# Kernel optimization log

Hardware: AMD Instinct MI355X
Metric: run time of the kernel (lower is better)

Reference implementation:

```python
import jax, jax.numpy as jnp
import numpy as np

NUM_NODES = 128
TEMPERATURE = 1.0
NEG = -1e30  # stand-in for -inf that is safe under softmax/grad


def setup_inputs() -> dict:
    key = jax.random.key(0)
    k1, k2, k3 = jax.random.split(key, 3)
    D, N = 1024, NUM_NODES
    P = jax.random.normal(k1, (N, N), jnp.float32)
    P = P.at[jnp.arange(N), jnp.arange(N)].set(-50.0)  # fill_diagonal_(-50)
    uniforms = jax.random.uniform(k2, (D, N), jnp.float32)       # categorical sampling draws
    gumbel_u = jax.random.uniform(k3, (D, 2, N, N), jnp.float32)  # gumbel-softmax base uniforms
    return {"P": P, "uniforms": uniforms, "gumbel_u": gumbel_u, "num_dags": D}


def reference(P, uniforms, gumbel_u, num_dags):
    N = P.shape[0]
    D = uniforms.shape[0]
    sigP = jax.nn.sigmoid(P)  # [N,N], shared across all dags

    # --- Phase 1: sequential node-ordering sampling (mask-based, fixed shapes) ---
    def step(active, u):
        # active: [D,N] bool, True = node still remaining
        masked = jnp.where(active[:, None, :], sigP[None, :, :], NEG)  # [D,N,N]
        row_max = masked.max(-1)                                       # max over remaining cols
        logits = jnp.where(active, (1.0 - row_max) / TEMPERATURE, NEG)
        probs = jax.nn.softmax(logits, axis=-1)                        # softmax over remaining rows
        cum = jnp.cumsum(probs, -1)
        cond = (cum >= u[:, None]) & active
        idx = jnp.argmax(cond, -1)
        last_active = (N - 1) - jnp.argmax(active[:, ::-1], -1)
        idx = jnp.where(cond.any(-1), idx, last_active)  # fp fallback
        active = active & (jnp.arange(N)[None, :] != idx[:, None])
        return active, idx

    active0 = jnp.ones((D, N), dtype=bool)
    _, order_T = jax.lax.scan(step, active0, uniforms.T)  # scan over N steps
    order = order_T.T  # [D,N]

    # --- Phase 2: permute, lower-triangular, gumbel-softmax, unpermute ---
    Ap = sigP[order[:, :, None], order[:, None, :]]  # [D,N,N] = sigP[order_i, order_j]
    tril_mask = jnp.tril(jnp.ones((N, N), dtype=bool), -1)
    A_low = jnp.where(tril_mask, Ap, 0.0)
    logA = jnp.where(tril_mask, jnp.log(jnp.where(tril_mask, Ap, 1.0)), NEG)
    log1mA = jnp.log1p(-A_low)
    logits2 = jnp.stack([logA, log1mA], axis=1)  # [D,2,N,N]
    g = -jnp.log(-jnp.log(gumbel_u + 1e-10) + 1e-10)
    y_soft = jax.nn.softmax(logits2 + g, axis=1)  # tau = 1 (torch default)
    am = jnp.argmax(y_soft, axis=1)  # [D,N,N]
    hard = (am[:, None, :, :] == jnp.arange(2)[None, :, None, None]).astype(y_soft.dtype)
    y = jax.lax.stop_gradient(hard - y_soft) + y_soft  # straight-through
    Y = y[:, 0]  # [D,N,N]

    # undo permutation: out[d, order[i], order[j]] = Y[d, i, j]
    inv = jnp.argsort(order, axis=-1)
    unperm = jax.vmap(lambda m, p: m[p][:, p])(Y, inv)
    return unperm.transpose(0, 2, 1), order
```

## Files before the change

kernel.cpp:

```cpp
#include <hip/hip_runtime.h>

#define NN 128
#define NEGF -1e30f
#define DELTA 1.5e-5f

__device__ __forceinline__ float dpp_scan_add(float x) {
    int v;
    v = __builtin_amdgcn_update_dpp(0, __float_as_int(x), 0x111, 0xf, 0xf, true);
    x += __int_as_float(v);
    v = __builtin_amdgcn_update_dpp(0, __float_as_int(x), 0x112, 0xf, 0xf, true);
    x += __int_as_float(v);
    v = __builtin_amdgcn_update_dpp(0, __float_as_int(x), 0x114, 0xf, 0xf, true);
    x += __int_as_float(v);
    v = __builtin_amdgcn_update_dpp(0, __float_as_int(x), 0x118, 0xf, 0xf, true);
    x += __int_as_float(v);
    v = __builtin_amdgcn_update_dpp(0, __float_as_int(x), 0x142, 0xa, 0xf, true);
    x += __int_as_float(v);
    v = __builtin_amdgcn_update_dpp(0, __float_as_int(x), 0x143, 0xc, 0xf, true);
    x += __int_as_float(v);
    return x;
}

__device__ __forceinline__ float dpp_scan_max(float x) {
    const int negi = __float_as_int(NEGF);
    int v;
    v = __builtin_amdgcn_update_dpp(negi, __float_as_int(x), 0x111, 0xf, 0xf, false);
    x = fmaxf(x, __int_as_float(v));
    v = __builtin_amdgcn_update_dpp(negi, __float_as_int(x), 0x112, 0xf, 0xf, false);
    x = fmaxf(x, __int_as_float(v));
    v = __builtin_amdgcn_update_dpp(negi, __float_as_int(x), 0x114, 0xf, 0xf, false);
    x = fmaxf(x, __int_as_float(v));
    v = __builtin_amdgcn_update_dpp(negi, __float_as_int(x), 0x118, 0xf, 0xf, false);
    x = fmaxf(x, __int_as_float(v));
    v = __builtin_amdgcn_update_dpp(negi, __float_as_int(x), 0x142, 0xa, 0xf, false);
    x = fmaxf(x, __int_as_float(v));
    v = __builtin_amdgcn_update_dpp(negi, __float_as_int(x), 0x143, 0xc, 0xf, false);
    x = fmaxf(x, __int_as_float(v));
    return x;
}

__device__ __forceinline__ float bcast63(float x) {
    return __int_as_float(__builtin_amdgcn_readlane(__float_as_int(x), 63));
}

__global__ void k_sig(const float* __restrict__ P, float* __restrict__ sigS) {
    int i = blockIdx.x * blockDim.x + threadIdx.x;
    if (i < NN * NN) {
        double p = (double)P[i];
        sigS[i] = (float)(1.0 / (1.0 + exp(-p)));
    }
}

__launch_bounds__(256)
__global__ void k_fused(const float* __restrict__ sigS,
                        const float* __restrict__ uniforms,
                        const float* __restrict__ G,
                        float* __restrict__ out0,
                        float* __restrict__ orderF, int D) {
    __shared__ float S[NN * NN];
    __shared__ int ordS[4 * NN];
    __shared__ unsigned char T8[NN * NN];
    const int tid = threadIdx.x;

    for (int k = 0; k < 16; ++k) {
        int idx4 = (k * 256 + tid) * 4;
        int r = idx4 >> 7, cb = idx4 & 127;
        float4 v = *reinterpret_cast<const float4*>(&sigS[idx4]);
        int x = r & 31;
        float4 w;
        switch (x & 3) {
            case 0: w = v; break;
            case 1: w = make_float4(v.y, v.x, v.w, v.z); break;
            case 2: w = make_float4(v.z, v.w, v.x, v.y); break;
            default: w = make_float4(v.w, v.z, v.y, v.x); break;
        }
        *reinterpret_cast<float4*>(&S[r * 128 + ((cb ^ x) & ~3)]) = w;
    }
    __syncthreads();

    const int lane = tid & 63;
    const int wv = tid >> 6;
    const int dag = blockIdx.x * 4 + wv;

    if (dag < D) {
        const int i0 = 2 * lane, i1 = 2 * lane + 1;
        const int x0 = i0 & 31, x1 = i1 & 31;
        const int q0 = x0 & 3, q1 = x1 & 3;
        float2 uu = *reinterpret_cast<const float2*>(&uniforms[dag * NN + i0]);

        unsigned long long mlo = ~0ull, mhi = ~0ull;

        float rm0 = NEGF, rm1 = NEGF;
        int rc0 = 0, rc1 = 0;
        for (int k = 0; k < 32; ++k) {
            int cb = 4 * ((k + lane) & 31);
            float4 a = *reinterpret_cast<const float4*>(&S[i0 * 128 + (cb ^ (x0 & ~3))]);
            float4 b = *reinterpret_cast<const float4*>(&S[i1 * 128 + (cb ^ (x1 & ~3))]);
            if (a.x > rm0) { rm0 = a.x; rc0 = cb | (0 ^ q0); }
            if (a.y > rm0) { rm0 = a.y; rc0 = cb | (1 ^ q0); }
            if (a.z > rm0) { rm0 = a.z; rc0 = cb | (2 ^ q0); }
            if (a.w > rm0) { rm0 = a.w; rc0 = cb | (3 ^ q0); }
            if (b.x > rm1) { rm1 = b.x; rc1 = cb | (0 ^ q1); }
            if (b.y > rm1) { rm1 = b.y; rc1 = cb | (1 ^ q1); }
            if (b.z > rm1) { rm1 = b.z; rc1 = cb | (2 ^ q1); }
            if (b.w > rm1) { rm1 = b.w; rc1 = cb | (3 ^ q1); }
        }

        float e0 = __expf(1.0f - rm0);
        float e1 = __expf(1.0f - rm1);

        #pragma unroll 1
        for (int t = 0; t < NN; ++t) {
            float usel = (t & 1) ? uu.y : uu.x;
            float ut = __int_as_float(__builtin_amdgcn_readlane(__float_as_int(usel), t >> 1));

            float incl = dpp_scan_add(e0 + e1);
            float T = bcast63(incl);
            float thr = ut * T;
            float cum1 = incl, cum0 = incl - e1;

            bool a0 = (e0 != 0.0f), a1 = (e1 != 0.0f);
            bool c0 = a0 && (cum0 >= thr);
            bool c1 = a1 && (cum1 >= thr);
            float mg = DELTA * T;
            bool amb = (a0 && fabsf(cum0 - thr) <= mg) || (a1 && fabsf(cum1 - thr) <= mg);

            unsigned long long b0 = __ballot(c0), b1 = __ballot(c1);
            unsigned long long ba = __ballot(amb);
            int lastActive = mhi ? (127 - __clzll(mhi)) : (63 - __clzll(mlo));

            int idx;
            if (__builtin_expect(ba != 0ull, 0)) {
                float l0 = 1.0f - rm0, l1v = 1.0f - rm1;
                float lvi = fmaxf(a0 ? l0 : NEGF, a1 ? l1v : NEGF);
                float lv = bcast63(dpp_scan_max(lvi));
                float f0 = a0 ? expf(l0 - lv) : 0.0f;
                float f1 = a1 ? expf(l1v - lv) : 0.0f;
                int mm = lane & 3;
                float s0 = __shfl(f0, mm), s1 = __shfl(f1, mm);
                #pragma unroll
                for (int k2 = 1; k2 < 16; ++k2) {
                    s0 += __shfl(f0, mm + 4 * k2);
                    s1 += __shfl(f1, mm + 4 * k2);
                }
                float A00 = __shfl(s0, 0), A01 = __shfl(s0, 1), A02 = __shfl(s0, 2), A03 = __shfl(s0, 3);
                float A10 = __shfl(s1, 0), A11 = __shfl(s1, 1), A12 = __shfl(s1, 2), A13 = __shfl(s1, 3);
                float tot = ((A00 + A10) + (A01 + A11)) + ((A02 + A12) + (A03 + A13));
                float s = 0.0f;
                int pick = -1;
                for (int j = 0; j < NN; ++j) {
                    float ej = __shfl((j & 1) ? f1 : f0, j >> 1);
                    float pj = ej / tot;
                    s += pj;
                    bool aj = (j < 64) ? ((mlo >> j) & 1ull) : ((mhi >> (j - 64)) & 1ull);
                    if (pick < 0 && aj && s >= ut) pick = j;
                }
                idx = (pick >= 0) ? pick : lastActive;
            } else {
                int f0i = b0 ? 2 * (__ffsll(b0) - 1) : 999;
                int f1i = b1 ? 2 * (__ffsll(b1) - 1) + 1 : 999;
                idx = min(f0i, f1i);
                if (idx == 999) idx = lastActive;
            }

            if (lane == 0) ordS[wv * NN + t] = idx;

            if (idx < 64) mlo &= ~(1ull << idx);
            else          mhi &= ~(1ull << (idx - 64));
            if (idx == i0) e0 = 0.0f;
            if (idx == i1) e1 = 0.0f;
            a0 = (e0 != 0.0f); a1 = (e1 != 0.0f);

            unsigned long long r0 = __ballot(a0 && (rc0 == idx));
            unsigned long long r1 = __ballot(a1 && (rc1 == idx));

            while (r0) {
                int L = __ffsll(r0) - 1; r0 &= r0 - 1;
                int row = 2 * L, xm = row & 31;
                float v0 = ((mlo >> lane) & 1) ? S[row * 128 + (lane ^ xm)] : NEGF;
                float v1 = ((mhi >> lane) & 1) ? S[row * 128 + ((lane + 64) ^ xm)] : NEGF;
                float m2 = bcast63(dpp_scan_max(fmaxf(v0, v1)));
                unsigned long long h0 = __ballot(v0 == m2);
                unsigned long long h1 = __ballot(v1 == m2);
                int nc = h0 ? (__ffsll(h0) - 1) : (64 + __ffsll(h1) - 1);
                if (lane == L) { rm0 = m2; rc0 = nc; e0 = __expf(1.0f - m2); }
            }
            while (r1) {
                int L = __ffsll(r1) - 1; r1 &= r1 - 1;
                int row = 2 * L + 1, xm = row & 31;
                float v0 = ((mlo >> lane) & 1) ? S[row * 128 + (lane ^ xm)] : NEGF;
                float v1 = ((mhi >> lane) & 1) ? S[row * 128 + ((lane + 64) ^ xm)] : NEGF;
                float m2 = bcast63(dpp_scan_max(fmaxf(v0, v1)));
                unsigned long long h0 = __ballot(v0 == m2);
                unsigned long long h1 = __ballot(v1 == m2);
                int nc = h0 ? (__ffsll(h0) - 1) : (64 + __ffsll(h1) - 1);
                if (lane == L) { rm1 = m2; rc1 = nc; e1 = __expf(1.0f - m2); }
            }
        }
    }
    __syncthreads();

    #pragma unroll
    for (int k = 0; k < 2; ++k) {
        int i = k * 256 + tid;
        int dg = blockIdx.x * 4 + (i >> 7);
        if (dg < D) orderF[(size_t)blockIdx.x * 512 + i] = (float)ordS[i];
    }

    for (int w = 0; w < 4; ++w) {
        const int d = blockIdx.x * 4 + w;
        if (d >= D) break;

        uint4 z = make_uint4(0, 0, 0, 0);
        #pragma unroll
        for (int k = 0; k < 4; ++k) ((uint4*)T8)[k * 256 + tid] = z;
        __syncthreads();

        const float* G0 = G + (size_t)d * 2 * NN * NN;
        const float* G1 = G0 + NN * NN;
        const int* pw = &ordS[w * NN];

        for (int base = 0; base < 8192; base += 2048) {
            float u0[8], u1[8], sg[8];
            int rr8[8], cc8[8];
            bool ok[8];
            #pragma unroll
            for (int j = 0; j < 8; ++j) {
                int k = base + j * 256 + tid;
                ok[j] = (k < 8128);
                if (ok[j]) {
                    float fr = sqrtf(8.0f * (float)k + 1.0f);
                    int r = (int)((1.0f + fr) * 0.5f);
                    if (r * (r - 1) / 2 > k) --r;
                    if ((r + 1) * r / 2 <= k) ++r;
                    int c = k - r * (r - 1) / 2;
                    rr8[j] = r; cc8[j] = c;
                    int idx = r * NN + c;
                    u0[j] = G0[idx];
                    u1[j] = G1[idx];
                    int prr = pw[r], pcc = pw[c];
                    sg[j] = S[prr * 128 + (pcc ^ (prr & 31))];
                }
            }
            #pragma unroll
            for (int j = 0; j < 8; ++j) {
                if (ok[j]) {
                    int prr = pw[rr8[j]], pcc = pw[cc8[j]];
                    float A = -__logf(u0[j] + 1e-10f) + 1e-10f;
                    float B = -__logf(u1[j] + 1e-10f) + 1e-10f;
                    T8[pcc * NN + (prr ^ (pcc & 124))] = (sg[j] * B >= (1.0f - sg[j]) * A) ? 1 : 0;
                }
            }
        }
        __syncthreads();

        float* od = out0 + (size_t)d * NN * NN;
        #pragma unroll
        for (int k = 0; k < 16; ++k) {
            int base = k * 1024 + tid * 4;
            int i = base >> 7, j = base & 127;
            const uchar4 v = *reinterpret_cast<const uchar4*>(&T8[i * NN + (j ^ (i & 124))]);
            float4 o;
            o.x = (float)v.x; o.y = (float)v.y; o.z = (float)v.z; o.w = (float)v.w;
            *reinterpret_cast<float4*>(&od[base]) = o;
        }
        __syncthreads();
    }
}

extern "C" void kernel_launch(void* const* d_in, const int* in_sizes, int n_in,
                              void* d_out, int out_size, void* d_ws, size_t ws_size,
                              hipStream_t stream) {
    const float* P        = (const float*)d_in[0];
    const float* uniforms = (const float*)d_in[1];
    const float* G        = (const float*)d_in[2];
    const int D = in_sizes[1] / NN;

    float* out0   = (float*)d_out;
    float* orderF = out0 + (size_t)D * NN * NN;
    float* sigS   = (float*)d_ws;

    k_sig<<<(NN * NN + 255) / 256, 256, 0, stream>>>(P, sigS);
    k_fused<<<(D + 3) / 4, 256, 0, stream>>>(sigS, uniforms, G, out0, orderF, D);
}
```

Before: 148.1 us.

## Give each wave its own DAG phase-2 tile and drop block-wide barriers

Phase 2 changes from all four waves cooperating on each DAG in turn, with __syncthreads between steps, to each wave handling its own DAG in a private 16KB T8 buffer. Waves no longer wait for the slowest wave's sampling phase before starting their gumbel and output work. LDS grows from about 82KB to about 131KB per block, which likely limits the kernel to one block per CU. Each wave also now does four times as many serial iterations, so latency hiding depends more on running waves independently.

```diff
diff --git a/kernel.cpp b/kernel.cpp
--- a/kernel.cpp
+++ b/kernel.cpp
@@ -58,8 +58,8 @@
                         float* __restrict__ out0,
                         float* __restrict__ orderF, int D) {
     __shared__ float S[NN * NN];
+    __shared__ unsigned char T8[4][NN * NN];
     __shared__ int ordS[4 * NN];
-    __shared__ unsigned char T8[NN * NN];
     const int tid = threadIdx.x;
 
     for (int k = 0; k < 16; ++k) {
@@ -81,8 +81,9 @@
     const int lane = tid & 63;
     const int wv = tid >> 6;
     const int dag = blockIdx.x * 4 + wv;
-
-    if (dag < D) {
+    if (dag >= D) return;
+
+    {
         const int i0 = 2 * lane, i1 = 2 * lane + 1;
         const int x0 = i0 & 31, x1 = i1 & 31;
         const int q0 = x0 & 3, q1 = x1 & 3;
@@ -198,73 +199,66 @@
             }
         }
     }
-    __syncthreads();
-
+
+    const int* pw = &ordS[wv * NN];
+    unsigned char* Tw = T8[wv];
+
+    {
+        float2 o = make_float2((float)pw[2 * lane], (float)pw[2 * lane + 1]);
+        *reinterpret_cast<float2*>(&orderF[(size_t)dag * NN + 2 * lane]) = o;
+    }
+
+    uint4 z = make_uint4(0, 0, 0, 0);
     #pragma unroll
-    for (int k = 0; k < 2; ++k) {
-        int i = k * 256 + tid;
-        int dg = blockIdx.x * 4 + (i >> 7);
-        if (dg < D) orderF[(size_t)blockIdx.x * 512 + i] = (float)ordS[i];
-    }
-
-    for (int w = 0; w < 4; ++w) {
-        const int d = blockIdx.x * 4 + w;
-        if (d >= D) break;
-
-        uint4 z = make_uint4(0, 0, 0, 0);
+    for (int k = 0; k < 16; ++k)
+        reinterpret_cast<uint4*>(Tw)[k * 64 + lane] = z;
+    asm volatile("s_waitcnt lgkmcnt(0)" ::: "memory");
+
+    const float* G0 = G + (size_t)dag * 2 * NN * NN;
+    const float* G1 = G0 + NN * NN;
+
+    for (int base = 0; base < 8192; base += 512) {
+        float u0[8], u1[8], sg[8];
+        int rr8[8], cc8[8];
+        bool ok[8];
         #pragma unroll
-        for (int k = 0; k < 4; ++k) ((uint4*)T8)[k * 256 + tid] = z;
-        __syncthreads();
-
-        const float* G0 = G + (size_t)d * 2 * NN * NN;
-        const float* G1 = G0 + NN * NN;
-        const int* pw = &ordS[w * NN];
-
-        for (int base = 0; base < 8192; base += 2048) {
-            float u0[8], u1[8], sg[8];
-            int rr8[8], cc8[8];
-            bool ok[8];
-            #pragma unroll
-            for (int j = 0; j < 8; ++j) {
-                int k = base + j * 256 + tid;
-                ok[j] = (k < 8128);
-                if (ok[j]) {
-                    float fr = sqrtf(8.0f * (float)k + 1.0f);
-                    int r = (int)((1.0f + fr) * 0.5f);
-                    if (r * (r - 1) / 2 > k) --r;
-                    if ((r + 1) * r / 2 <= k) ++r;
-                    int c = k - r * (r - 1) / 2;
-                    rr8[j] = r; cc8[j] = c;
-                    int idx = r * NN + c;
-                    u0[j] = G0[idx];
-                    u1[j] = G1[idx];
-                    int prr = pw[r], pcc = pw[c];
-                    sg[j] = S[prr * 128 + (pcc ^ (prr & 31))];
-                }
-            }
-            #pragma unroll
-            for (int j = 0; j < 8; ++j) {
-                if (ok[j]) {
-                    int prr = pw[rr8[j]], pcc = pw[cc8[j]];
-                    float A = -__logf(u0[j] + 1e-10f) + 1e-10f;
-                    float B = -__logf(u1[j] + 1e-10f) + 1e-10f;
-                    T8[pcc * NN + (prr ^ (pcc & 124))] = (sg[j] * B >= (1.0f - sg[j]) * A) ? 1 : 0;
-                }
-            }
-        }
-        __syncthreads();
-
-        float* od = out0 + (size_t)d * NN * NN;
+        for (int j = 0; j < 8; ++j) {
+            int k = base + j * 64 + lane;
+            ok[j] = (k < 8128);
+            if (ok[j]) {
+                float fr = sqrtf(8.0f * (float)k + 1.0f);
+                int r = (int)((1.0f + fr) * 0.5f);
+                if (r * (r - 1) / 2 > k) --r;
+                if ((r + 1) * r / 2 <= k) ++r;
+                int c = k - r * (r - 1) / 2;
+                rr8[j] = r; cc8[j] = c;
+                int idx = r * NN + c;
+                u0[j] = G0[idx];
+                u1[j] = G1[idx];
+                int prr = pw[r], pcc = pw[c];
+                sg[j] = S[prr * 128 + (pcc ^ (prr & 31))];
+            }
+        }
         #pragma unroll
-        for (int k = 0; k < 16; ++k) {
-            int base = k * 1024 + tid * 4;
-            int i = base >> 7, j = base & 127;
-            const uchar4 v = *reinterpret_cast<const uchar4*>(&T8[i * NN + (j ^ (i & 124))]);
-            float4 o;
-            o.x = (float)v.x; o.y = (float)v.y; o.z = (float)v.z; o.w = (float)v.w;
-            *reinterpret_cast<float4*>(&od[base]) = o;
-        }
-        __syncthreads();
+        for (int j = 0; j < 8; ++j) {
+            if (ok[j]) {
+                int prr = pw[rr8[j]], pcc = pw[cc8[j]];
+                float A = -__logf(u0[j] + 1e-10f) + 1e-10f;
+                float B = -__logf(u1[j] + 1e-10f) + 1e-10f;
+                Tw[pcc * NN + (prr ^ (pcc & 124))] = (sg[j] * B >= (1.0f - sg[j]) * A) ? 1 : 0;
+            }
+        }
+    }
+
+    float* od = out0 + (size_t)dag * NN * NN;
+    #pragma unroll 4
+    for (int k = 0; k < 64; ++k) {
+        int base = k * 256 + lane * 4;
+        int i = base >> 7, j = base & 127;
+        const uchar4 v = *reinterpret_cast<const uchar4*>(&Tw[i * NN + (j ^ (i & 124))]);
+        float4 o;
+        o.x = (float)v.x; o.y = (float)v.y; o.z = (float)v.z; o.w = (float)v.w;
+        *reinterpret_cast<float4*>(&od[base]) = o;
     }
 }
 
```

Result: slower. 157.8 us (+6.6%).
